# Kernel optimization log

Measured on AMD Instinct MI355X. Metric: run time of the kernel, lower is better.

The kernel has to match this reference:

```python
import jax, jax.numpy as jnp
import numpy as np

VAR_W = 1.0
DIST_W = 1.0
M_VAR = 0.1
M_DIST = 1.5
IGNORE = 255
C = 16  # static upper bound on instance ids (labels 1..C; 0 = background)


def setup_inputs() -> dict:
    key = jax.random.key(0)
    ks = jax.random.split(key, 6)
    shapes = [(16, 1, 1024, 1024), (16, 1, 512, 512), (16, 1, 256, 256)]
    d = {}
    for idx, s in enumerate(shapes):
        d[f"featmap{idx}"] = jax.random.normal(ks[idx], s, dtype=jnp.float32)
        d[f"gt{idx}"] = jax.random.randint(ks[3 + idx], s, 0, C + 1, dtype=jnp.int32)
    return d


def _push_pull(feats, gts):
    B = feats[0].shape[0]
    nseg = B * (C + 1)
    b_off = (jnp.arange(B, dtype=jnp.int32) * (C + 1))[:, None]  # [B,1]

    segs, valids, ffs = [], [], []
    tot_sum = jnp.zeros((nseg,), dtype=feats[0].dtype)
    tot_cnt = jnp.zeros((nseg,), dtype=feats[0].dtype)
    # pass 1: per (batch, instance) sums / counts pooled over all scales
    for f, g in zip(feats, gts):
        ff = f.reshape(B, -1)            # [B, N_s]
        gg = g.reshape(B, -1)
        valid = (gg >= 1) & (gg <= C) & (gg < IGNORE)
        lab = jnp.where(valid, gg, 0)
        seg = (lab + b_off).reshape(-1)  # [B*N_s], segment id = b*(C+1)+label
        vf = valid.reshape(-1).astype(ff.dtype)
        tot_sum = tot_sum + jax.ops.segment_sum(jnp.where(valid, ff, 0.0).reshape(-1), seg, num_segments=nseg)
        tot_cnt = tot_cnt + jax.ops.segment_sum(vf, seg, num_segments=nseg)
        segs.append(seg); valids.append(valid); ffs.append(ff)

    mean = tot_sum / jnp.maximum(tot_cnt, 1.0)  # [nseg] per-(b,instance) mean over all scales

    # pass 2: pull loss -- per-scale mean of clamp(|x - mean| - margin_var, 0)^2, summed over scales
    pull_seg = jnp.zeros((nseg,), dtype=feats[0].dtype)
    for ff, seg, valid in zip(ffs, segs, valids):
        m_pix = mean[seg].reshape(ff.shape)
        val = jnp.where(valid, jnp.square(jnp.maximum(jnp.abs(ff - m_pix) - M_VAR, 0.0)), 0.0)
        ssum = jax.ops.segment_sum(val.reshape(-1), seg, num_segments=nseg)
        scnt = jax.ops.segment_sum(valid.reshape(-1).astype(ff.dtype), seg, num_segments=nseg)
        pull_seg = pull_seg + jnp.where(scnt > 0, ssum / jnp.maximum(scnt, 1.0), 0.0)

    present = tot_cnt.reshape(B, C + 1)[:, 1:] > 0        # [B,C]
    pull_i = pull_seg.reshape(B, C + 1)[:, 1:]            # [B,C]
    n_pull = jnp.maximum(present.sum(), 1).astype(pull_i.dtype)
    pull_loss = jnp.sum(jnp.where(present, pull_i, 0.0)) / n_pull * VAR_W

    # push loss: all ordered pairs (i,j), i!=j, both present in that batch element
    m = mean.reshape(B, C + 1)[:, 1:]                     # [B,C]
    diff = jnp.abs(m[:, :, None] - m[:, None, :])         # [B,C,C]
    pv = jnp.square(jnp.maximum(2.0 * M_DIST - diff, 0.0))
    pm = present[:, :, None] & present[:, None, :] & ~jnp.eye(C, dtype=bool)[None]
    n_push = jnp.maximum(pm.sum(), 1).astype(pv.dtype)
    push_loss = jnp.sum(jnp.where(pm, pv, 0.0)) / n_push * DIST_W

    return push_loss + pull_loss


def reference(featmap0, featmap1, featmap2, gt0, gt1, gt2):
    return _push_pull([featmap0, featmap1, featmap2], [gt0, gt1, gt2])
```

## Files before the change

kernel.cpp:

```cpp
#include <hip/hip_runtime.h>


#define NSEG 272
#define M_VAR 0.1f
#define TWO_M_DIST 3.0f

#define SUB0 48
#define SUB1 12
#define SUB2 3
#define GRID_BLOCKS (16 * (SUB0 + SUB1 + SUB2))

__device__ __forceinline__ void gatomic_add(float* p, float v) {
  __hip_atomic_fetch_add(p, v, __ATOMIC_RELAXED, __HIP_MEMORY_SCOPE_AGENT);
}

struct Sel {
  const float4* f; const int4* g;
  int vbase, vend, stride, scale, batch;
};

__device__ __forceinline__ Sel pick(
    int b, int t,
    const float4* f0, const int4* g0,
    const float4* f1, const int4* g1,
    const float4* f2, const int4* g2) {
  Sel s;
  if (b < 16 * SUB0) {
    int batch = b / SUB0, sub = b - batch * SUB0;
    s.f = f0; s.g = g0; s.scale = 0; s.batch = batch;
    s.vbase = batch * 262144 + sub * 256 + t;
    s.vend  = (batch + 1) * 262144;
    s.stride = SUB0 * 256;
  } else if (b < 16 * (SUB0 + SUB1)) {
    int lb = b - 16 * SUB0; int batch = lb / SUB1, sub = lb - batch * SUB1;
    s.f = f1; s.g = g1; s.scale = 1; s.batch = batch;
    s.vbase = batch * 65536 + sub * 256 + t;
    s.vend  = (batch + 1) * 65536;
    s.stride = SUB1 * 256;
  } else {
    int lb = b - 16 * (SUB0 + SUB1); int batch = lb / SUB2, sub = lb - batch * SUB2;
    s.f = f2; s.g = g2; s.scale = 2; s.batch = batch;
    s.vbase = batch * 16384 + sub * 256 + t;
    s.vend  = (batch + 1) * 16384;
    s.stride = SUB2 * 256;
  }
  return s;
}

__global__ __launch_bounds__(256, 4) void pass1_kernel(
    const float4* __restrict__ f0, const int4* __restrict__ g0,
    const float4* __restrict__ f1, const int4* __restrict__ g1,
    const float4* __restrict__ f2, const int4* __restrict__ g2,
    float* __restrict__ tot_sum,
    float* __restrict__ cnt)
{
  const int t = threadIdx.x;
  Sel s = pick(blockIdx.x, t, f0, g0, f1, g1, f2, g2);

  float sum[17];
  int   cn[17];
  #pragma unroll
  for (int l = 1; l <= 16; ++l) { sum[l] = 0.f; cn[l] = 0; }

  int v = s.vbase;
  float4 fv = s.f[v];
  int4   gv = s.g[v];
  while (true) {
    int vn = v + s.stride;
    bool more = (vn < s.vend);
    float4 fn; int4 gn;
    if (more) { fn = s.f[vn]; gn = s.g[vn]; }

    #pragma unroll
    for (int l = 1; l <= 16; ++l) {
      sum[l] += (gv.x == l) ? fv.x : 0.f;  cn[l] += (gv.x == l) ? 1 : 0;
      sum[l] += (gv.y == l) ? fv.y : 0.f;  cn[l] += (gv.y == l) ? 1 : 0;
      sum[l] += (gv.z == l) ? fv.z : 0.f;  cn[l] += (gv.z == l) ? 1 : 0;
      sum[l] += (gv.w == l) ? fv.w : 0.f;  cn[l] += (gv.w == l) ? 1 : 0;
    }

    if (!more) break;
    v = vn; fv = fn; gv = gn;
  }

  __shared__ float rsum[4][16];
  __shared__ float rcnt[4][16];
  const int lane = t & 63, wave = t >> 6;
  #pragma unroll
  for (int l = 1; l <= 16; ++l) {
    float sv = sum[l];
    float cv = (float)cn[l];
    #pragma unroll
    for (int o = 32; o > 0; o >>= 1) {
      sv += __shfl_down(sv, o);
      cv += __shfl_down(cv, o);
    }
    if (lane == 0) { rsum[wave][l - 1] = sv; rcnt[wave][l - 1] = cv; }
  }
  __syncthreads();

  if (t < 16) {
    float sv = rsum[0][t] + rsum[1][t] + rsum[2][t] + rsum[3][t];
    float cv = rcnt[0][t] + rcnt[1][t] + rcnt[2][t] + rcnt[3][t];
    if (cv != 0.f) {
      gatomic_add(&tot_sum[s.batch * 17 + 1 + t], sv);
      gatomic_add(&cnt[s.scale * NSEG + s.batch * 17 + 1 + t], cv);
    }
  }
}

__global__ __launch_bounds__(256, 4) void pass2_kernel(
    const float4* __restrict__ f0, const int4* __restrict__ g0,
    const float4* __restrict__ f1, const int4* __restrict__ g1,
    const float4* __restrict__ f2, const int4* __restrict__ g2,
    const float* __restrict__ tot_sum,
    const float* __restrict__ cnt,
    float* __restrict__ pull_acc)
{
  __shared__ float2 s_mi[17];
  const int t = threadIdx.x;
  Sel s = pick(blockIdx.x, t, f0, g0, f1, g1, f2, g2);

  if (t < 17) {
    int i = s.batch * 17 + t;
    float c = cnt[i] + cnt[NSEG + i] + cnt[2 * NSEG + i];
    float mean = tot_sum[i] / fmaxf(c, 1.f);
    float cs = cnt[s.scale * NSEG + i];
    float inv = (t >= 1 && cs > 0.f) ? (1.f / cs) : 0.f;
    s_mi[t] = make_float2(mean, inv);
  }
  __syncthreads();

  float acc = 0.f;
  int v = s.vbase;
  float4 fv = s.f[v];
  int4   gv = s.g[v];
  while (true) {
    int vn = v + s.stride;
    bool more = (vn < s.vend);
    float4 fn; int4 gn;
    if (more) { fn = s.f[vn]; gn = s.g[vn]; }

    {
      float2 mi = s_mi[min((unsigned)gv.x, 16u)];
      float d = fmaxf(fabsf(fv.x - mi.x) - M_VAR, 0.f);
      acc += d * d * mi.y;
    }
    {
      float2 mi = s_mi[min((unsigned)gv.y, 16u)];
      float d = fmaxf(fabsf(fv.y - mi.x) - M_VAR, 0.f);
      acc += d * d * mi.y;
    }
    {
      float2 mi = s_mi[min((unsigned)gv.z, 16u)];
      float d = fmaxf(fabsf(fv.z - mi.x) - M_VAR, 0.f);
      acc += d * d * mi.y;
    }
    {
      float2 mi = s_mi[min((unsigned)gv.w, 16u)];
      float d = fmaxf(fabsf(fv.w - mi.x) - M_VAR, 0.f);
      acc += d * d * mi.y;
    }

    if (!more) break;
    v = vn; fv = fn; gv = gn;
  }

  #pragma unroll
  for (int o = 32; o > 0; o >>= 1) acc += __shfl_down(acc, o);
  __shared__ float racc[4];
  const int lane = t & 63, wave = t >> 6;
  if (lane == 0) racc[wave] = acc;
  __syncthreads();
  if (t == 0) gatomic_add(pull_acc, racc[0] + racc[1] + racc[2] + racc[3]);
}

__global__ __launch_bounds__(256) void finalize_kernel(
    const float* __restrict__ tot_sum, const float* __restrict__ cnt,
    const float* __restrict__ pull_acc, float* __restrict__ out) {
  __shared__ float s_mean[NSEG];
  __shared__ unsigned char s_pres[NSEG];
  const int t = threadIdx.x;
  for (int i = t; i < NSEG; i += 256) {
    float c = cnt[i] + cnt[NSEG + i] + cnt[2 * NSEG + i];
    s_pres[i] = (c > 0.f) ? 1 : 0;
    s_mean[i] = tot_sum[i] / fmaxf(c, 1.f);
  }
  __syncthreads();

  float pull_n = 0.f, push_v = 0.f, push_n = 0.f;

  for (int i = t; i < NSEG; i += 256) {
    int lab = i - (i / 17) * 17;
    if (lab >= 1 && s_pres[i]) pull_n += 1.f;
  }

  {
    int b = t >> 4, ii = t & 15;
    int si = b * 17 + ii + 1;
    if (s_pres[si]) {
      float mi = s_mean[si];
      for (int j = 0; j < 16; ++j) {
        if (j == ii) continue;
        int sj = b * 17 + j + 1;
        if (s_pres[sj]) {
          float d = fmaxf(TWO_M_DIST - fabsf(mi - s_mean[sj]), 0.f);
          push_v += d * d;
          push_n += 1.f;
        }
      }
    }
  }

  #pragma unroll
  for (int o = 32; o > 0; o >>= 1) {
    pull_n += __shfl_down(pull_n, o);
    push_v += __shfl_down(push_v, o);
    push_n += __shfl_down(push_n, o);
  }
  __shared__ float r[4][3];
  int wave = t >> 6;
  if ((t & 63) == 0) { r[wave][0] = pull_n; r[wave][1] = push_v; r[wave][2] = push_n; }
  __syncthreads();
  if (t == 0) {
    float PN = 0, SV = 0, SN = 0;
    for (int w = 0; w < 4; ++w) { PN += r[w][0]; SV += r[w][1]; SN += r[w][2]; }
    out[0] = pull_acc[0] / fmaxf(PN, 1.f) + SV / fmaxf(SN, 1.f);
  }
}

extern "C" void kernel_launch(void* const* d_in, const int* in_sizes, int n_in,
                              void* d_out, int out_size, void* d_ws, size_t ws_size,
                              hipStream_t stream) {
  const float4* f0 = (const float4*)d_in[0];
  const int4*   g0 = (const int4*)  d_in[1];
  const float4* f1 = (const float4*)d_in[2];
  const int4*   g1 = (const int4*)  d_in[3];
  const float4* f2 = (const float4*)d_in[4];
  const int4*   g2 = (const int4*)  d_in[5];

  float* ws       = (float*)d_ws;
  float* tot_sum  = ws;
  float* cnt      = ws + NSEG;
  float* pull_acc = ws + 4 * NSEG;

  hipMemsetAsync(d_ws, 0, (4 * NSEG + 1) * sizeof(float), stream);
  pass1_kernel<<<GRID_BLOCKS, 256, 0, stream>>>(f0, g0, f1, g1, f2, g2, tot_sum, cnt);
  pass2_kernel<<<GRID_BLOCKS, 256, 0, stream>>>(f0, g0, f1, g1, f2, g2, tot_sum, cnt, pull_acc);
  finalize_kernel<<<1, 256, 0, stream>>>(tot_sum, cnt, pull_acc, (float*)d_out);
}
```

Baseline: 229.1 us.

## Replace atomics and memset with per-block partials, fuse finalize via last-block

Pass 1 now writes per-block partial sums and counts to workspace instead of global atomics. Pass 2 reduces those partials itself to get the means, and the last block to finish (found with an atomic counter) computes the final loss, so the memset and the separate finalize launch are gone. Per-label counts now use wave ballot plus popcount instead of per-thread integer adds, cutting register use. The grid is retuned to a fixed 16 iterations per thread, which removes the bounds check in the loop. The trade-off is that every pull block redundantly re-reduces the partials, and correctness depends on the fixed problem sizes.

```diff
diff --git a/kernel.cpp b/kernel.cpp
--- a/kernel.cpp
+++ b/kernel.cpp
@@ -1,212 +1,219 @@
 #include <hip/hip_runtime.h>
 
 
-#define NSEG 272
 #define M_VAR 0.1f
 #define TWO_M_DIST 3.0f
 
-#define SUB0 48
-#define SUB1 12
-#define SUB2 3
-#define GRID_BLOCKS (16 * (SUB0 + SUB1 + SUB2))
-
-__device__ __forceinline__ void gatomic_add(float* p, float v) {
-  __hip_atomic_fetch_add(p, v, __ATOMIC_RELAXED, __HIP_MEMORY_SCOPE_AGENT);
-}
+#define SUB0 64
+#define SUB1 16
+#define SUB2 4
+#define PER_BATCH (SUB0 + SUB1 + SUB2)
+#define NBATCH 16
+#define GRID_BLOCKS (NBATCH * PER_BATCH)
+#define NITER 16
+
+#define OFF_PSUM  0
+#define OFF_PCNT  (GRID_BLOCKS * 16)
+#define OFF_GMEAN (2 * GRID_BLOCKS * 16)
+#define OFF_GCNT  (OFF_GMEAN + 256)
+#define OFF_PULL  (OFF_GCNT + 256)
+#define OFF_CTR   (OFF_PULL + GRID_BLOCKS)
 
 struct Sel {
   const float4* f; const int4* g;
-  int vbase, vend, stride, scale, batch;
+  int vbase, stride, batch, j;
 };
 
 __device__ __forceinline__ Sel pick(
-    int b, int t,
+    int bid, int t,
     const float4* f0, const int4* g0,
     const float4* f1, const int4* g1,
     const float4* f2, const int4* g2) {
   Sel s;
-  if (b < 16 * SUB0) {
-    int batch = b / SUB0, sub = b - batch * SUB0;
-    s.f = f0; s.g = g0; s.scale = 0; s.batch = batch;
-    s.vbase = batch * 262144 + sub * 256 + t;
-    s.vend  = (batch + 1) * 262144;
-    s.stride = SUB0 * 256;
-  } else if (b < 16 * (SUB0 + SUB1)) {
-    int lb = b - 16 * SUB0; int batch = lb / SUB1, sub = lb - batch * SUB1;
-    s.f = f1; s.g = g1; s.scale = 1; s.batch = batch;
-    s.vbase = batch * 65536 + sub * 256 + t;
-    s.vend  = (batch + 1) * 65536;
-    s.stride = SUB1 * 256;
+  s.batch = bid / PER_BATCH;
+  s.j = bid - s.batch * PER_BATCH;
+  if (s.j < SUB0) {
+    s.f = f0; s.g = g0;
+    s.vbase = s.batch * 262144 + s.j * 256 + t;             s.stride = SUB0 * 256;
+  } else if (s.j < SUB0 + SUB1) {
+    s.f = f1; s.g = g1; int sub = s.j - SUB0;
+    s.vbase = s.batch * 65536 + sub * 256 + t;              s.stride = SUB1 * 256;
   } else {
-    int lb = b - 16 * (SUB0 + SUB1); int batch = lb / SUB2, sub = lb - batch * SUB2;
-    s.f = f2; s.g = g2; s.scale = 2; s.batch = batch;
-    s.vbase = batch * 16384 + sub * 256 + t;
-    s.vend  = (batch + 1) * 16384;
-    s.stride = SUB2 * 256;
+    s.f = f2; s.g = g2; int sub = s.j - SUB0 - SUB1;
+    s.vbase = s.batch * 16384 + sub * 256 + t;              s.stride = SUB2 * 256;
   }
   return s;
 }
 
-__global__ __launch_bounds__(256, 4) void pass1_kernel(
+__global__ __launch_bounds__(256, 4) void hist_kernel(
     const float4* __restrict__ f0, const int4* __restrict__ g0,
     const float4* __restrict__ f1, const int4* __restrict__ g1,
     const float4* __restrict__ f2, const int4* __restrict__ g2,
-    float* __restrict__ tot_sum,
-    float* __restrict__ cnt)
+    float* __restrict__ ws)
 {
-  const int t = threadIdx.x;
-  Sel s = pick(blockIdx.x, t, f0, g0, f1, g1, f2, g2);
-
-  float sum[17];
-  int   cn[17];
-  #pragma unroll
-  for (int l = 1; l <= 16; ++l) { sum[l] = 0.f; cn[l] = 0; }
+  const int t = threadIdx.x, bid = blockIdx.x;
+  if (bid == 0 && t == 0) *((unsigned*)(ws + OFF_CTR)) = 0u;
+
+  Sel s = pick(bid, t, f0, g0, f1, g1, f2, g2);
+
+  float sum[16];
+  int   cnt[16];
+  #pragma unroll
+  for (int l = 0; l < 16; ++l) { sum[l] = 0.f; cnt[l] = 0; }
 
   int v = s.vbase;
   float4 fv = s.f[v];
   int4   gv = s.g[v];
-  while (true) {
+  #pragma unroll 1
+  for (int it = 0; it < NITER; ++it) {
     int vn = v + s.stride;
-    bool more = (vn < s.vend);
     float4 fn; int4 gn;
-    if (more) { fn = s.f[vn]; gn = s.g[vn]; }
+    if (it + 1 < NITER) { fn = s.f[vn]; gn = s.g[vn]; }
 
     #pragma unroll
-    for (int l = 1; l <= 16; ++l) {
-      sum[l] += (gv.x == l) ? fv.x : 0.f;  cn[l] += (gv.x == l) ? 1 : 0;
-      sum[l] += (gv.y == l) ? fv.y : 0.f;  cn[l] += (gv.y == l) ? 1 : 0;
-      sum[l] += (gv.z == l) ? fv.z : 0.f;  cn[l] += (gv.z == l) ? 1 : 0;
-      sum[l] += (gv.w == l) ? fv.w : 0.f;  cn[l] += (gv.w == l) ? 1 : 0;
-    }
-
-    if (!more) break;
+    for (int l = 0; l < 16; ++l) {
+      bool cx = (gv.x == l + 1); sum[l] += cx ? fv.x : 0.f;
+      bool cy = (gv.y == l + 1); sum[l] += cy ? fv.y : 0.f;
+      bool cz = (gv.z == l + 1); sum[l] += cz ? fv.z : 0.f;
+      bool cw = (gv.w == l + 1); sum[l] += cw ? fv.w : 0.f;
+      cnt[l] += (int)__popcll(__ballot(cx)) + (int)__popcll(__ballot(cy))
+              + (int)__popcll(__ballot(cz)) + (int)__popcll(__ballot(cw));
+    }
     v = vn; fv = fn; gv = gn;
   }
 
-  __shared__ float rsum[4][16];
-  __shared__ float rcnt[4][16];
+  __shared__ float rs[4][16];
+  __shared__ float rc[4][16];
   const int lane = t & 63, wave = t >> 6;
   #pragma unroll
-  for (int l = 1; l <= 16; ++l) {
+  for (int l = 0; l < 16; ++l) {
     float sv = sum[l];
-    float cv = (float)cn[l];
     #pragma unroll
-    for (int o = 32; o > 0; o >>= 1) {
-      sv += __shfl_down(sv, o);
-      cv += __shfl_down(cv, o);
-    }
-    if (lane == 0) { rsum[wave][l - 1] = sv; rcnt[wave][l - 1] = cv; }
-  }
-  __syncthreads();
-
+    for (int o = 32; o > 0; o >>= 1) sv += __shfl_down(sv, o);
+    if (lane == 0) rs[wave][l] = sv;
+  }
+  if (lane == 0) {
+    #pragma unroll
+    for (int l = 0; l < 16; ++l) rc[wave][l] = (float)cnt[l];
+  }
+  __syncthreads();
   if (t < 16) {
-    float sv = rsum[0][t] + rsum[1][t] + rsum[2][t] + rsum[3][t];
-    float cv = rcnt[0][t] + rcnt[1][t] + rcnt[2][t] + rcnt[3][t];
-    if (cv != 0.f) {
-      gatomic_add(&tot_sum[s.batch * 17 + 1 + t], sv);
-      gatomic_add(&cnt[s.scale * NSEG + s.batch * 17 + 1 + t], cv);
-    }
-  }
-}
-
-__global__ __launch_bounds__(256, 4) void pass2_kernel(
+    ws[OFF_PSUM + bid * 16 + t] = rs[0][t] + rs[1][t] + rs[2][t] + rs[3][t];
+    ws[OFF_PCNT + bid * 16 + t] = rc[0][t] + rc[1][t] + rc[2][t] + rc[3][t];
+  }
+}
+
+__global__ __launch_bounds__(256, 4) void pull_kernel(
     const float4* __restrict__ f0, const int4* __restrict__ g0,
     const float4* __restrict__ f1, const int4* __restrict__ g1,
     const float4* __restrict__ f2, const int4* __restrict__ g2,
-    const float* __restrict__ tot_sum,
-    const float* __restrict__ cnt,
-    float* __restrict__ pull_acc)
+    float* __restrict__ ws, float* __restrict__ out)
 {
+  const int t = threadIdx.x, bid = blockIdx.x;
+  Sel s = pick(bid, t, f0, g0, f1, g1, f2, g2);
+  const int myscale = (s.j < SUB0) ? 0 : ((s.j < SUB0 + SUB1) ? 1 : 2);
+
+  __shared__ float ls[16][16], lc[16][16], lm[16][16];
   __shared__ float2 s_mi[17];
-  const int t = threadIdx.x;
-  Sel s = pick(blockIdx.x, t, f0, g0, f1, g1, f2, g2);
-
-  if (t < 17) {
-    int i = s.batch * 17 + t;
-    float c = cnt[i] + cnt[NSEG + i] + cnt[2 * NSEG + i];
-    float mean = tot_sum[i] / fmaxf(c, 1.f);
-    float cs = cnt[s.scale * NSEG + i];
-    float inv = (t >= 1 && cs > 0.f) ? (1.f / cs) : 0.f;
-    s_mi[t] = make_float2(mean, inv);
+  {
+    const int label = t & 15, k = t >> 4;
+    float ts = 0.f, tc = 0.f, mc = 0.f;
+    const float* psum = ws + OFF_PSUM + s.batch * PER_BATCH * 16;
+    const float* pcnt = ws + OFF_PCNT + s.batch * PER_BATCH * 16;
+    for (int jj = k; jj < PER_BATCH; jj += 16) {
+      float sv = psum[jj * 16 + label];
+      float cv = pcnt[jj * 16 + label];
+      ts += sv; tc += cv;
+      int js = (jj < SUB0) ? 0 : ((jj < SUB0 + SUB1) ? 1 : 2);
+      mc += (js == myscale) ? cv : 0.f;
+    }
+    ls[k][label] = ts; lc[k][label] = tc; lm[k][label] = mc;
+  }
+  __syncthreads();
+  if (t == 0) s_mi[0] = make_float2(0.f, 0.f);
+  if (t < 16) {
+    float ts = 0.f, tc = 0.f, mc = 0.f;
+    #pragma unroll 1
+    for (int k = 0; k < 16; ++k) { ts += ls[k][t]; tc += lc[k][t]; mc += lm[k][t]; }
+    float mean = ts / fmaxf(tc, 1.f);
+    s_mi[1 + t] = make_float2(mean, (mc > 0.f) ? (1.f / mc) : 0.f);
+    if (s.j == 0) {
+      ws[OFF_GMEAN + s.batch * 16 + t] = mean;
+      ws[OFF_GCNT  + s.batch * 16 + t] = tc;
+    }
   }
   __syncthreads();
 
   float acc = 0.f;
-  int v = s.vbase;
-  float4 fv = s.f[v];
-  int4   gv = s.g[v];
-  while (true) {
-    int vn = v + s.stride;
-    bool more = (vn < s.vend);
-    float4 fn; int4 gn;
-    if (more) { fn = s.f[vn]; gn = s.g[vn]; }
-
-    {
-      float2 mi = s_mi[min((unsigned)gv.x, 16u)];
-      float d = fmaxf(fabsf(fv.x - mi.x) - M_VAR, 0.f);
-      acc += d * d * mi.y;
-    }
-    {
-      float2 mi = s_mi[min((unsigned)gv.y, 16u)];
-      float d = fmaxf(fabsf(fv.y - mi.x) - M_VAR, 0.f);
-      acc += d * d * mi.y;
-    }
-    {
-      float2 mi = s_mi[min((unsigned)gv.z, 16u)];
-      float d = fmaxf(fabsf(fv.z - mi.x) - M_VAR, 0.f);
-      acc += d * d * mi.y;
-    }
-    {
-      float2 mi = s_mi[min((unsigned)gv.w, 16u)];
-      float d = fmaxf(fabsf(fv.w - mi.x) - M_VAR, 0.f);
-      acc += d * d * mi.y;
-    }
-
-    if (!more) break;
-    v = vn; fv = fn; gv = gn;
-  }
-
+  {
+    int v = s.vbase;
+    float4 fv = s.f[v];
+    int4   gv = s.g[v];
+    #pragma unroll 1
+    for (int it = 0; it < NITER; ++it) {
+      int vn = v + s.stride;
+      float4 fn; int4 gn;
+      if (it + 1 < NITER) { fn = s.f[vn]; gn = s.g[vn]; }
+      {
+        float2 a = s_mi[min((unsigned)gv.x, 16u)];
+        float d = fmaxf(fabsf(fv.x - a.x) - M_VAR, 0.f); acc += d * d * a.y;
+      }
+      {
+        float2 a = s_mi[min((unsigned)gv.y, 16u)];
+        float d = fmaxf(fabsf(fv.y - a.x) - M_VAR, 0.f); acc += d * d * a.y;
+      }
+      {
+        float2 a = s_mi[min((unsigned)gv.z, 16u)];
+        float d = fmaxf(fabsf(fv.z - a.x) - M_VAR, 0.f); acc += d * d * a.y;
+      }
+      {
+        float2 a = s_mi[min((unsigned)gv.w, 16u)];
+        float d = fmaxf(fabsf(fv.w - a.x) - M_VAR, 0.f); acc += d * d * a.y;
+      }
+      v = vn; fv = fn; gv = gn;
+    }
+  }
   #pragma unroll
   for (int o = 32; o > 0; o >>= 1) acc += __shfl_down(acc, o);
   __shared__ float racc[4];
-  const int lane = t & 63, wave = t >> 6;
-  if (lane == 0) racc[wave] = acc;
-  __syncthreads();
-  if (t == 0) gatomic_add(pull_acc, racc[0] + racc[1] + racc[2] + racc[3]);
-}
-
-__global__ __launch_bounds__(256) void finalize_kernel(
-    const float* __restrict__ tot_sum, const float* __restrict__ cnt,
-    const float* __restrict__ pull_acc, float* __restrict__ out) {
-  __shared__ float s_mean[NSEG];
-  __shared__ unsigned char s_pres[NSEG];
-  const int t = threadIdx.x;
-  for (int i = t; i < NSEG; i += 256) {
-    float c = cnt[i] + cnt[NSEG + i] + cnt[2 * NSEG + i];
-    s_pres[i] = (c > 0.f) ? 1 : 0;
-    s_mean[i] = tot_sum[i] / fmaxf(c, 1.f);
-  }
-  __syncthreads();
-
-  float pull_n = 0.f, push_v = 0.f, push_n = 0.f;
-
-  for (int i = t; i < NSEG; i += 256) {
-    int lab = i - (i / 17) * 17;
-    if (lab >= 1 && s_pres[i]) pull_n += 1.f;
-  }
-
+  if ((t & 63) == 0) racc[t >> 6] = acc;
+  __syncthreads();
+  if (t == 0) ws[OFF_PULL + bid] = racc[0] + racc[1] + racc[2] + racc[3];
+
+  __shared__ int s_last;
+  if (t == 0) {
+    __threadfence();
+    unsigned old = __hip_atomic_fetch_add((unsigned*)(ws + OFF_CTR), 1u,
+                                          __ATOMIC_ACQ_REL, __HIP_MEMORY_SCOPE_AGENT);
+    s_last = (old == GRID_BLOCKS - 1) ? 1 : 0;
+  }
+  __syncthreads();
+  if (!s_last) return;
+
+  __shared__ float s_mean[256];
+  __shared__ float s_pres[256];
+  {
+    float cval = ws[OFF_GCNT + t];
+    s_mean[t] = ws[OFF_GMEAN + t];
+    s_pres[t] = (cval > 0.f) ? 1.f : 0.f;
+  }
+  __syncthreads();
+
+  float pull_v = 0.f;
+  for (int i = t; i < GRID_BLOCKS; i += 256) pull_v += ws[OFF_PULL + i];
+
+  float pull_n = s_pres[t];
+  float push_v = 0.f, push_n = 0.f;
   {
     int b = t >> 4, ii = t & 15;
-    int si = b * 17 + ii + 1;
-    if (s_pres[si]) {
-      float mi = s_mean[si];
-      for (int j = 0; j < 16; ++j) {
-        if (j == ii) continue;
-        int sj = b * 17 + j + 1;
-        if (s_pres[sj]) {
+    if (s_pres[t] > 0.f) {
+      float mi = s_mean[t];
+      for (int jj = 0; jj < 16; ++jj) {
+        if (jj == ii) continue;
+        int sj = (b << 4) | jj;
+        if (s_pres[sj] > 0.f) {
           float d = fmaxf(TWO_M_DIST - fabsf(mi - s_mean[sj]), 0.f);
-          push_v += d * d;
-          push_n += 1.f;
+          push_v += d * d; push_n += 1.f;
         }
       }
     }
@@ -214,18 +221,19 @@
 
   #pragma unroll
   for (int o = 32; o > 0; o >>= 1) {
+    pull_v += __shfl_down(pull_v, o);
     pull_n += __shfl_down(pull_n, o);
     push_v += __shfl_down(push_v, o);
     push_n += __shfl_down(push_n, o);
   }
-  __shared__ float r[4][3];
+  __shared__ float r[4][4];
   int wave = t >> 6;
-  if ((t & 63) == 0) { r[wave][0] = pull_n; r[wave][1] = push_v; r[wave][2] = push_n; }
+  if ((t & 63) == 0) { r[wave][0] = pull_v; r[wave][1] = pull_n; r[wave][2] = push_v; r[wave][3] = push_n; }
   __syncthreads();
   if (t == 0) {
-    float PN = 0, SV = 0, SN = 0;
-    for (int w = 0; w < 4; ++w) { PN += r[w][0]; SV += r[w][1]; SN += r[w][2]; }
-    out[0] = pull_acc[0] / fmaxf(PN, 1.f) + SV / fmaxf(SN, 1.f);
+    float PV = 0, PN = 0, SV = 0, SN = 0;
+    for (int w = 0; w < 4; ++w) { PV += r[w][0]; PN += r[w][1]; SV += r[w][2]; SN += r[w][3]; }
+    out[0] = PV / fmaxf(PN, 1.f) + SV / fmaxf(SN, 1.f);
   }
 }
 
@@ -238,14 +246,9 @@
   const int4*   g1 = (const int4*)  d_in[3];
   const float4* f2 = (const float4*)d_in[4];
   const int4*   g2 = (const int4*)  d_in[5];
-
-  float* ws       = (float*)d_ws;
-  float* tot_sum  = ws;
-  float* cnt      = ws + NSEG;
-  float* pull_acc = ws + 4 * NSEG;
-
-  hipMemsetAsync(d_ws, 0, (4 * NSEG + 1) * sizeof(float), stream);
-  pass1_kernel<<<GRID_BLOCKS, 256, 0, stream>>>(f0, g0, f1, g1, f2, g2, tot_sum, cnt);
-  pass2_kernel<<<GRID_BLOCKS, 256, 0, stream>>>(f0, g0, f1, g1, f2, g2, tot_sum, cnt, pull_acc);
-  finalize_kernel<<<1, 256, 0, stream>>>(tot_sum, cnt, pull_acc, (float*)d_out);
-}
+  float* ws  = (float*)d_ws;
+  float* out = (float*)d_out;
+
+  hist_kernel<<<GRID_BLOCKS, 256, 0, stream>>>(f0, g0, f1, g1, f2, g2, ws);
+  pull_kernel<<<GRID_BLOCKS, 256, 0, stream>>>(f0, g0, f1, g1, f2, g2, ws, out);
+}
```

Measured after the change: 291.2 us. 27.1% more time.
